# Kernel tuning notes

Hardware: AMD Instinct MI355X
Metric: run time of the kernel (lower is better)

The kernel has to match this reference:

```python
import jax, jax.numpy as jnp
import numpy as np

EPS = 1e-5

def conv1x1(x, w, b):
    # x: [B,Cin,H,W], w: [Cout,Cin], b: [Cout]
    return jnp.einsum('oi,bihw->bohw', w, x) + b[None, :, None, None]

def self_attention(x, qw, qb, kw, kb, vw, vb, fw, fb):
    B, C, H, W = x.shape
    hid = qw.shape[0]
    q = conv1x1(x, qw, qb).reshape(B, hid, H * W).transpose(0, 2, 1)   # [B,HW,hid]
    k = conv1x1(x, kw, kb).reshape(B, hid, H * W)                      # [B,hid,HW]
    v = conv1x1(x, vw, vb).reshape(B, C, H * W)                        # [B,C,HW]
    attn = jax.nn.softmax(jnp.einsum('bnh,bhm->bnm', q, k), axis=-1)   # [B,HW,HW]
    z = jnp.einsum('bnm,bcm->bnc', attn, v)                            # [B,HW,C]
    # faithful to torch .view(B,C,H,W) on contiguous [B,HW,C]: raw reshape, no transpose
    z = z.reshape(B, C, H, W)
    return conv1x1(z * x, fw, fb) + x

def group_norm_per_channel(y, gw, gb):
    # GroupNorm(num_groups == num_channels): per-channel instance norm, biased var
    mean = y.mean(axis=(2, 3), keepdims=True)
    var = ((y - mean) ** 2).mean(axis=(2, 3), keepdims=True)
    yn = (y - mean) * jax.lax.rsqrt(var + EPS)
    return yn * gw[None, :, None, None] + gb[None, :, None, None]

def setup_inputs() -> dict:
    key = jax.random.key(0)
    ks = jax.random.split(key, 32)
    B, C, H, W = 4, 64, 64, 64
    hid, att = 64, 64
    d = {}
    d['x'] = jax.random.normal(ks[0], (B, C, H, W), jnp.float32)
    d['h'] = jax.random.normal(ks[1], (B, hid, H, W), jnp.float32)
    d['c'] = jax.random.normal(ks[2], (B, hid, H, W), jnp.float32)
    i = 3
    for pre, cin in (('ax', C), ('ah', hid)):
        for nm, cout in (('q', att), ('k', att), ('v', cin), ('f', cin)):
            d[f'{pre}_{nm}w'] = jax.random.normal(ks[i], (cout, cin), jnp.float32) * 0.05; i += 1
            d[f'{pre}_{nm}b'] = jax.random.normal(ks[i], (cout,), jnp.float32) * 0.05; i += 1
    d['conv_w'] = jax.random.normal(ks[i], (4 * hid, C + hid, 3, 3), jnp.float32) * 0.05; i += 1
    d['conv_b'] = jax.random.normal(ks[i], (4 * hid,), jnp.float32) * 0.05; i += 1
    d['gn_w'] = jnp.ones((4 * hid,), jnp.float32)
    d['gn_b'] = jnp.zeros((4 * hid,), jnp.float32)
    return d

def reference(x, h, c,
              ax_qw, ax_qb, ax_kw, ax_kb, ax_vw, ax_vb, ax_fw, ax_fb,
              ah_qw, ah_qb, ah_kw, ah_kb, ah_vw, ah_vb, ah_fw, ah_fb,
              conv_w, conv_b, gn_w, gn_b):
    hid = h.shape[1]
    xa = self_attention(x, ax_qw, ax_qb, ax_kw, ax_kb, ax_vw, ax_vb, ax_fw, ax_fb)
    ha = self_attention(h, ah_qw, ah_qb, ah_kw, ah_kb, ah_vw, ah_vb, ah_fw, ah_fb)
    combined = jnp.concatenate([xa, ha], axis=1)
    y = jax.lax.conv_general_dilated(
        combined, conv_w, window_strides=(1, 1), padding=[(1, 1), (1, 1)],
        dimension_numbers=('NCHW', 'OIHW', 'NCHW')) + conv_b[None, :, None, None]
    y = group_norm_per_channel(y, gn_w, gn_b)
    i, f, o, g = jnp.split(y, 4, axis=1)
    i = jax.nn.sigmoid(i); f = jax.nn.sigmoid(f); o = jax.nn.sigmoid(o); g = jnp.tanh(g)
    c_next = f * c + i * g
    h_next = o * jnp.tanh(c_next)
    return jnp.stack([h_next, c_next])  # [2,B,hid,H,W]
```

## Files before the change

### kernel.cpp

```cpp
#include <hip/hip_runtime.h>
#include <hip/hip_bf16.h>


typedef __hip_bfloat16 bf16;
typedef const __hip_bfloat16* bfp;
typedef short bf16x8 __attribute__((ext_vector_type(8)));
typedef short short4v __attribute__((ext_vector_type(4)));
typedef float f32x4 __attribute__((ext_vector_type(4)));
typedef unsigned int u32x4 __attribute__((ext_vector_type(4)));

#define SM_SHIFT 12.0f
#define LOG2E      1.4426950408889634f
#define SM_BIAS2  -17.312340490667562f
#define SM_CLAMP2  86.561702453337805f

__device__ __forceinline__ float ldf(const void* p, long i, int f32) {
    return f32 ? ((const float*)p)[i]
               : __bfloat162float(((const bf16*)p)[i]);
}
__device__ __forceinline__ short f2bf(float f) {
    bf16 h = __float2bfloat16(f);
    return *reinterpret_cast<short*>(&h);
}

__device__ __forceinline__ int sniff_f32(const void* xr)
{
    int lane = threadIdx.x & 63;
    unsigned long long v = ((const unsigned long long*)xr)[lane];
    int ok = 0;
#pragma unroll
    for (int i = 0; i < 4; ++i) {
        int e = (int)((v >> (16 * i + 7)) & 0xFF);
        ok += (e >= 100 && e <= 141);
    }
    ok += __shfl_xor(ok, 1, 64);
    ok += __shfl_xor(ok, 2, 64);
    ok += __shfl_xor(ok, 4, 64);
    ok += __shfl_xor(ok, 8, 64);
    ok += __shfl_xor(ok, 16, 64);
    ok += __shfl_xor(ok, 32, 64);
    return ok < 200;
}

__global__ __launch_bounds__(256) void qkv_kernel(
    const void* __restrict__ Xx, const void* __restrict__ Xh,
    const void* __restrict__ qwx, const void* __restrict__ qbx,
    const void* __restrict__ kwx, const void* __restrict__ kbx,
    const void* __restrict__ vwx, const void* __restrict__ vbx,
    const void* __restrict__ qwh, const void* __restrict__ qbh,
    const void* __restrict__ kwh, const void* __restrict__ kbh,
    const void* __restrict__ vwh, const void* __restrict__ vbh,
    bf16* __restrict__ Qx, bf16* __restrict__ Kx, bf16* __restrict__ Vtx,
    bf16* __restrict__ Qh, bf16* __restrict__ Kh, bf16* __restrict__ Vth,
    const void* __restrict__ cw, bf16* __restrict__ Wt,
    float* __restrict__ gacc, int qkvN)
{
    int bx = blockIdx.x;
    int tid = threadIdx.x;
    int f32 = sniff_f32(Xx);
    if (bx >= qkvN) {
        if (bx == qkvN) {
            for (int j = 0; j < 8; ++j)
                gacc[tid * 8 + j] = 0.f;
        }
        int wi = (bx - qkvN) * 256 + tid;
        int tap = wi >> 15;
        int rem = wi & 32767;
        int oc = rem >> 7, ic = rem & 127;
        Wt[wi] = __float2bfloat16(ldf(cw, ((long)oc * 128 + ic) * 9 + tap, f32));
        return;
    }
    __shared__ __align__(16) short xt[64][72];
    __shared__ __align__(16) short wq[64][72];
    __shared__ __align__(16) short wk[64][72];
    __shared__ __align__(16) short wv[64][72];
    int ab  = (bx >> 8) & 1;
    int idx = bx & 255;
    int b = idx >> 6;
    int n0 = (idx & 63) * 64;
    int wave = tid >> 6, lane = tid & 63;
    int q = lane >> 4, l15 = lane & 15;

    const void* X = ab ? Xh : Xx;
    const void* qw = ab ? qwh : qwx; const void* qb = ab ? qbh : qbx;
    const void* kw = ab ? kwh : kwx; const void* kb = ab ? kbh : kbx;
    const void* vw = ab ? vwh : vwx; const void* vb = ab ? vbh : vbx;
    short* Qg  = (short*)(ab ? Qh  : Qx)  + (long)b * 262144;
    short* Kg  = (short*)(ab ? Kh  : Kx)  + (long)b * 262144;
    short* Vtg = (short*)(ab ? Vth : Vtx) + (long)b * 262144;

    if (!f32) {
        const short* q16 = (const short*)qw;
        const short* k16 = (const short*)kw;
        const short* v16 = (const short*)vw;
        for (int rep = 0; rep < 2; ++rep) {
            int j8 = (rep * 256 + tid) * 8;
            *(bf16x8*)&wq[j8 >> 6][j8 & 63] = *(const bf16x8*)(q16 + j8);
            *(bf16x8*)&wk[j8 >> 6][j8 & 63] = *(const bf16x8*)(k16 + j8);
            *(bf16x8*)&wv[j8 >> 6][j8 & 63] = *(const bf16x8*)(v16 + j8);
        }
    } else {
        for (int rep = 0; rep < 16; ++rep) {
            int j = rep * 256 + tid;
            int i = j >> 6, cc = j & 63;
            wq[i][cc] = f2bf(((const float*)qw)[j]);
            wk[i][cc] = f2bf(((const float*)kw)[j]);
            wv[i][cc] = f2bf(((const float*)vw)[j]);
        }
    }
    long xbase = (long)b * 262144;
    for (int rep = 0; rep < 16; ++rep) {
        int c = rep * 4 + (tid >> 6);
        int p = tid & 63;
        xt[p][c] = f2bf(ldf(X, xbase + (long)c * 4096 + n0 + p, f32));
    }
    __syncthreads();

    bf16x8 a0 = *(const bf16x8*)&xt[wave * 16 + l15][q * 8];
    bf16x8 a1 = *(const bf16x8*)&xt[wave * 16 + l15][32 + q * 8];

    for (int ct = 0; ct < 4; ++ct) {
        bf16x8 bq0 = *(const bf16x8*)&wq[ct * 16 + l15][q * 8];
        bf16x8 bq1 = *(const bf16x8*)&wq[ct * 16 + l15][32 + q * 8];
        f32x4 z = (f32x4){0.f, 0.f, 0.f, 0.f};
        z = __builtin_amdgcn_mfma_f32_16x16x32_bf16(a0, bq0, z, 0, 0, 0);
        z = __builtin_amdgcn_mfma_f32_16x16x32_bf16(a1, bq1, z, 0, 0, 0);
        float bias = ldf(qb, ct * 16 + l15, f32);
        for (int reg = 0; reg < 4; ++reg)
            Qg[(long)(n0 + wave * 16 + q * 4 + reg) * 64 + ct * 16 + l15] =
                f2bf(z[reg] + bias);
    }
    for (int ct = 0; ct < 4; ++ct) {
        bf16x8 bk0 = *(const bf16x8*)&wk[ct * 16 + l15][q * 8];
        bf16x8 bk1 = *(const bf16x8*)&wk[ct * 16 + l15][32 + q * 8];
        f32x4 z = (f32x4){0.f, 0.f, 0.f, 0.f};
        z = __builtin_amdgcn_mfma_f32_16x16x32_bf16(a0, bk0, z, 0, 0, 0);
        z = __builtin_amdgcn_mfma_f32_16x16x32_bf16(a1, bk1, z, 0, 0, 0);
        float bias = ldf(kb, ct * 16 + l15, f32);
        for (int reg = 0; reg < 4; ++reg)
            Kg[(long)(n0 + wave * 16 + q * 4 + reg) * 64 + ct * 16 + l15] =
                f2bf(z[reg] + bias);
    }
    bf16x8 av0 = *(const bf16x8*)&wv[wave * 16 + l15][q * 8];
    bf16x8 av1 = *(const bf16x8*)&wv[wave * 16 + l15][32 + q * 8];
    for (int ct = 0; ct < 4; ++ct) {
        bf16x8 bx0 = *(const bf16x8*)&xt[ct * 16 + l15][q * 8];
        bf16x8 bx1 = *(const bf16x8*)&xt[ct * 16 + l15][32 + q * 8];
        f32x4 z = (f32x4){0.f, 0.f, 0.f, 0.f};
        z = __builtin_amdgcn_mfma_f32_16x16x32_bf16(av0, bx0, z, 0, 0, 0);
        z = __builtin_amdgcn_mfma_f32_16x16x32_bf16(av1, bx1, z, 0, 0, 0);
        for (int reg = 0; reg < 4; ++reg) {
            int c_out = wave * 16 + q * 4 + reg;
            float bias = ldf(vb, c_out, f32);
            Vtg[(long)c_out * 4096 + n0 + ct * 16 + l15] = f2bf(z[reg] + bias);
        }
    }
}

__global__ __launch_bounds__(256, 2) void attn_kernel(
    bfp Qx, bfp Kx, bfp Vtx, bf16* Ox,
    bfp Qh, bfp Kh, bfp Vth, bf16* Oh,
    float* __restrict__ lw, int split)
{
    __shared__ __align__(16) short ks [2][64][64];
    __shared__ __align__(16) short vts[2][64][64];
    int tid = threadIdx.x;
    int wave = tid >> 6, lane = tid & 63;
    int q = lane >> 4, l15 = lane & 15;
    int idx = blockIdx.x & 255;
    int ab, half, mstart, ntile;
    if (split) {
        ab = blockIdx.x >> 9; half = (blockIdx.x >> 8) & 1;
        mstart = half * 2048; ntile = 32;
    } else {
        ab = blockIdx.x >> 8; half = 0; mstart = 0; ntile = 64;
    }
    int b = idx >> 6;
    int rt = idx & 63;
    int n0 = rt * 64 + wave * 16;
    const short* Qb  = (const short*)(ab ? Qh  : Qx)  + (long)b * 262144;
    const short* Kb  = (const short*)(ab ? Kh  : Kx)  + (long)b * 262144;
    const short* Vtb = (const short*)(ab ? Vth : Vtx) + (long)b * 262144;
    short* Ob = (short*)(ab ? Oh : Ox) + (long)half * (1l << 20) + (long)b * 262144;

    bf16x8 aq0 = *(const bf16x8*)(Qb + (long)(n0 + l15) * 64 + q * 8);
    bf16x8 aq1 = *(const bf16x8*)(Qb + (long)(n0 + l15) * 64 + 32 + q * 8);

    f32x4 acc_o[4];
    for (int ct = 0; ct < 4; ++ct) acc_o[ct] = (f32x4){0.f, 0.f, 0.f, 0.f};
    float l_acc = 0.f;

    int swp = (l15 >> 1) & 7;
    int c0 = (q ^ swp) << 3;
    int c1 = ((q + 4) ^ swp) << 3;
    int sw_s = (tid >> 4) & 7;
    int cs = (((tid & 7) ^ sw_s)) << 3;

    int r0 = tid >> 3, r1 = r0 + 32;
    int sr0 = (((r0 >> 5) + (((r0 >> 2) & 1) << 1)) << 4)
            | (((r0 >> 3) & 3) << 2) | (r0 & 3);
    int sr1 = (((r1 >> 5) + (((r1 >> 2) & 1) << 1)) << 4)
            | (((r1 >> 3) & 3) << 2) | (r1 & 3);
    int cs0 = (((tid & 7) ^ ((sr0 >> 1) & 7))) << 3;
    int cs1 = (((tid & 7) ^ ((sr1 >> 1) & 7))) << 3;

    bf16x8 pk0 = *(const bf16x8*)(Kb + (long)(mstart + r0) * 64 + (tid & 7) * 8);
    bf16x8 pk1 = *(const bf16x8*)(Kb + (long)(mstart + r1) * 64 + (tid & 7) * 8);
    bf16x8 pv0 = *(const bf16x8*)(Vtb + (long)r0 * 4096 + mstart + (tid & 7) * 8);
    bf16x8 pv1 = *(const bf16x8*)(Vtb + (long)r1 * 4096 + mstart + (tid & 7) * 8);

    for (int it = 0; it < ntile; ++it) {
        int buf = it & 1;
        *(bf16x8*)&ks[buf][sr0][cs0] = pk0;
        *(bf16x8*)&ks[buf][sr1][cs1] = pk1;
        *(bf16x8*)&vts[buf][r0][cs]  = pv0;
        *(bf16x8*)&vts[buf][r1][cs]  = pv1;
        __syncthreads();
        if (it + 1 < ntile) {
            long m = (long)mstart + (long)(it + 1) * 64;
            pk0 = *(const bf16x8*)(Kb + (m + r0) * 64 + (tid & 7) * 8);
            pk1 = *(const bf16x8*)(Kb + (m + r1) * 64 + (tid & 7) * 8);
            pv0 = *(const bf16x8*)(Vtb + (long)r0 * 4096 + m + (tid & 7) * 8);
            pv1 = *(const bf16x8*)(Vtb + (long)r1 * 4096 + m + (tid & 7) * 8);
        }

        f32x4 s[4];
#pragma unroll
        for (int t = 0; t < 4; ++t) {
            const short* krow = &ks[buf][t * 16 + l15][0];
            bf16x8 ak0 = *(const bf16x8*)(krow + c0);
            bf16x8 ak1 = *(const bf16x8*)(krow + c1);
            f32x4 z = (f32x4){0.f, 0.f, 0.f, 0.f};
            z    = __builtin_amdgcn_mfma_f32_16x16x32_bf16(ak0, aq0, z, 0, 0, 0);
            s[t] = __builtin_amdgcn_mfma_f32_16x16x32_bf16(ak1, aq1, z, 0, 0, 0);
        }

        unsigned P32[8];
        float lt = 0.f;
#pragma unroll
        for (int t = 0; t < 4; ++t) {
            float p0 = __builtin_amdgcn_exp2f(
                fminf(fmaf(s[t][0], LOG2E, SM_BIAS2), SM_CLAMP2));
            float p1 = __builtin_amdgcn_exp2f(
                fminf(fmaf(s[t][1], LOG2E, SM_BIAS2), SM_CLAMP2));
            float p2 = __builtin_amdgcn_exp2f(
                fminf(fmaf(s[t][2], LOG2E, SM_BIAS2), SM_CLAMP2));
            float p3 = __builtin_amdgcn_exp2f(
                fminf(fmaf(s[t][3], LOG2E, SM_BIAS2), SM_CLAMP2));
            lt += (p0 + p1) + (p2 + p3);
            P32[t * 2] = (unsigned)(unsigned short)f2bf(p0)
                       | ((unsigned)(unsigned short)f2bf(p1) << 16);
            P32[t * 2 + 1] = (unsigned)(unsigned short)f2bf(p2)
                           | ((unsigned)(unsigned short)f2bf(p3) << 16);
        }
        l_acc += lt;

        u32x4 B0v = (u32x4){P32[0], P32[1], P32[4], P32[5]};
        u32x4 B1v = (u32x4){P32[2], P32[3], P32[6], P32[7]};
        bf16x8 bp0 = __builtin_bit_cast(bf16x8, B0v);
        bf16x8 bp1 = __builtin_bit_cast(bf16x8, B1v);

        for (int ct = 0; ct < 4; ++ct) {
            const short* vrow = &vts[buf][ct * 16 + l15][0];
            bf16x8 av0 = *(const bf16x8*)(vrow + c0);
            bf16x8 av1 = *(const bf16x8*)(vrow + c1);
            acc_o[ct] = __builtin_amdgcn_mfma_f32_16x16x32_bf16(av0, bp0, acc_o[ct], 0, 0, 0);
            acc_o[ct] = __builtin_amdgcn_mfma_f32_16x16x32_bf16(av1, bp1, acc_o[ct], 0, 0, 0);
        }
    }

    l_acc += __shfl_xor(l_acc, 16, 64);
    l_acc += __shfl_xor(l_acc, 32, 64);

    if (split) {
        if (lane < 16) {
            lw[(long)ab * 32768 + (long)half * 16384
               + (long)b * 4096 + n0 + lane] = l_acc;
        }
        for (int ct = 0; ct < 4; ++ct) {
            short* dst = Ob + (long)(n0 + l15) * 64 + ct * 16 + q * 4;
            dst[0] = f2bf(acc_o[ct][0]);
            dst[1] = f2bf(acc_o[ct][1]);
            dst[2] = f2bf(acc_o[ct][2]);
            dst[3] = f2bf(acc_o[ct][3]);
        }
    } else {
        float iln = 1.f / l_acc;
        for (int ct = 0; ct < 4; ++ct) {
            short* dst = Ob + (long)(n0 + l15) * 64 + ct * 16 + q * 4;
            dst[0] = f2bf(acc_o[ct][0] * iln);
            dst[1] = f2bf(acc_o[ct][1] * iln);
            dst[2] = f2bf(acc_o[ct][2] * iln);
            dst[3] = f2bf(acc_o[ct][3] * iln);
        }
    }
}

__global__ __launch_bounds__(256) void attnout_kernel(
    bfp Ox, const void* __restrict__ Xx,
    const void* __restrict__ fwx, const void* __restrict__ fbx,
    bf16* __restrict__ outx,
    bfp Oh, const void* __restrict__ Xh,
    const void* __restrict__ fwh, const void* __restrict__ fbh,
    bf16* __restrict__ outh,
    const float* __restrict__ lw, int split)
{
    __shared__ __align__(16) short fwt[64][72];
    __shared__ __align__(16) short at [64][72];
    int f32 = sniff_f32(Xx);
    int ab  = blockIdx.x >> 8;
    int idx = blockIdx.x & 255;
    int b = idx >> 6;
    int h = idx & 63;
    int tid = threadIdx.x;
    int wave = tid >> 6, lane = tid & 63;
    int q = lane >> 4, l15 = lane & 15;
    bfp O = ab ? Oh : Ox;
    const void* X = ab ? Xh : Xx;
    const void* fw = ab ? fwh : fwx;
    const void* fb = ab ? fbh : fbx;
    bf16* out = ab ? outh : outx;

    if (!f32) {
        const short* f16p = (const short*)fw;
        for (int rep = 0; rep < 2; ++rep) {
            int j8 = (rep * 256 + tid) * 8;
            *(bf16x8*)&fwt[j8 >> 6][j8 & 63] = *(const bf16x8*)(f16p + j8);
        }
    } else {
        for (int rep = 0; rep < 16; ++rep) {
            int j = rep * 256 + tid;
            fwt[j >> 6][j & 63] = f2bf(((const float*)fw)[j]);
        }
    }
    const bf16* Ob0 = O + (long)b * 262144;
    const bf16* Ob1 = Ob0 + (1l << 20);
    const float* lp0 = lw + (long)ab * 32768 + (long)b * 4096;
    const float* lp1 = lp0 + 16384;
    long xbase = (long)b * 262144;
    {
        int w = tid & 63;
        for (int rep = 0; rep < 16; ++rep) {
            int cn = rep * 4 + (tid >> 6);
            int n = cn * 64 + h;
            float o;
            if (split) {
                float iln = 1.f / (lp0[n] + lp1[n]);
                o = (__bfloat162float(Ob0[(long)n * 64 + w]) +
                     __bfloat162float(Ob1[(long)n * 64 + w])) * iln;
            } else {
                o = __bfloat162float(Ob0[(long)n * 64 + w]);
            }
            float prod = o * ldf(X, xbase + (long)cn * 4096 + h * 64 + w, f32);
            at[w][cn] = f2bf(prod);
        }
    }
    __syncthreads();
    bf16x8 a0 = *(const bf16x8*)&fwt[wave * 16 + l15][q * 8];
    bf16x8 a1 = *(const bf16x8*)&fwt[wave * 16 + l15][32 + q * 8];
    short* outp = (short*)out;
    for (int nt = 0; nt < 4; ++nt) {
        bf16x8 b0 = *(const bf16x8*)&at[nt * 16 + l15][q * 8];
        bf16x8 b1 = *(const bf16x8*)&at[nt * 16 + l15][32 + q * 8];
        f32x4 z = (f32x4){0.f, 0.f, 0.f, 0.f};
        z = __builtin_amdgcn_mfma_f32_16x16x32_bf16(a0, b0, z, 0, 0, 0);
        z = __builtin_amdgcn_mfma_f32_16x16x32_bf16(a1, b1, z, 0, 0, 0);
        int w = nt * 16 + l15;
        short4v o4;
        for (int reg = 0; reg < 4; ++reg) {
            int o = wave * 16 + q * 4 + reg;
            float v = z[reg] + ldf(fb, o, f32) +
                      ldf(X, xbase + (long)o * 4096 + h * 64 + w, f32);
            o4[reg] = f2bf(v);
        }
        *(short4v*)(outp + (((long)(b * 64 + h) * 64 + w) * 64 + wave * 16 + q * 4)) = o4;
    }
}

__global__ __launch_bounds__(256) void conv3x3_kernel(
    bfp xa, bfp ha, bfp Wt, const void* __restrict__ cb,
    bf16* __restrict__ y, float* __restrict__ gacc,
    const void* __restrict__ xraw)
{
    __shared__ __align__(16) short in_s[3][66][136];
    int f32 = sniff_f32(xraw);
    int bx = blockIdx.x;
    int b = bx >> 7;
    int rem = bx & 127;
    int h = rem >> 1;
    int halfoc = rem & 1;
    int tid = threadIdx.x;
    int wave = tid >> 6, lane = tid & 63;
    int q = lane >> 4, l15 = lane & 15;

    const short* xab = (const short*)xa + (long)b * 262144;
    const short* hab = (const short*)ha + (long)b * 262144;
    const bf16x8 zv = {0, 0, 0, 0, 0, 0, 0, 0};
    for (int r = 0; r < 3; ++r) {
        int gy = h + r - 1;
        bool valid = (gy >= 0) && (gy < 64);
        for (int s = 0; s < 2; ++s) {
            int strip = s * 256 + tid;
            int w = strip >> 3;
            int c8 = (strip & 7) * 8;
            bf16x8 vx = zv, vh = zv;
            if (valid) {
                vx = *(const bf16x8*)(xab + ((long)gy * 64 + w) * 64 + c8);
                vh = *(const bf16x8*)(hab + ((long)gy * 64 + w) * 64 + c8);
            }
            *(bf16x8*)&in_s[r][w + 1][c8]      = vx;
            *(bf16x8*)&in_s[r][w + 1][64 + c8] = vh;
        }
    }
    if (tid < 96) {
        int r = tid / 32;
        int rest = tid % 32;
        int col = (rest & 1) ? 65 : 0;
        int c8 = (rest >> 1) * 8;
        *(bf16x8*)&in_s[r][col][c8] = zv;
    }
    __syncthreads();

    int oc0 = halfoc * 128 + wave * 32;
    f32x4 acc[2][4];
    for (int mt = 0; mt < 2; ++mt)
        for (int nt = 0; nt < 4; ++nt)
            acc[mt][nt] = (f32x4){0.f, 0.f, 0.f, 0.f};

    const short* Wb = (const short*)Wt;
    for (int tap = 0; tap < 9; ++tap) {
        int dy = tap / 3, dx = tap - dy * 3;
        for (int kc = 0; kc < 4; ++kc) {
            bf16x8 afrag[2];
            for (int mt = 0; mt < 2; ++mt)
                afrag[mt] = *(const bf16x8*)(
                    Wb + ((long)tap * 256 + oc0 + mt * 16 + l15) * 128 + kc * 32 + q * 8);
            for (int nt = 0; nt < 4; ++nt) {
                bf16x8 bfrag = *(const bf16x8*)&in_s[dy][nt * 16 + l15 + dx][kc * 32 + q * 8];
                for (int mt = 0; mt < 2; ++mt)
                    acc[mt][nt] = __builtin_amdgcn_mfma_f32_16x16x32_bf16(
                        afrag[mt], bfrag, acc[mt][nt], 0, 0, 0);
            }
        }
    }

    long ybase = (long)b * 1048576 + (long)h * 64;
    for (int mt = 0; mt < 2; ++mt) {
        for (int reg = 0; reg < 4; ++reg) {
            int oc = oc0 + mt * 16 + q * 4 + reg;
            float bias = ldf(cb, oc, f32);
            float s = 0.f, s2 = 0.f;
            for (int nt = 0; nt < 4; ++nt) {
                float v = acc[mt][nt][reg] + bias;
                ((short*)y)[ybase + (long)oc * 4096 + nt * 16 + l15] = f2bf(v);
                s += v; s2 = fmaf(v, v, s2);
            }
            s  += __shfl_xor(s,  1, 64);  s2 += __shfl_xor(s2, 1, 64);
            s  += __shfl_xor(s,  2, 64);  s2 += __shfl_xor(s2, 2, 64);
            s  += __shfl_xor(s,  4, 64);  s2 += __shfl_xor(s2, 4, 64);
            s  += __shfl_xor(s,  8, 64);  s2 += __shfl_xor(s2, 8, 64);
            if (l15 == 0) {
                atomicAdd(&gacc[b * 256 + oc], s);
                atomicAdd(&gacc[1024 + b * 256 + oc], s2);
            }
        }
    }
}

__global__ __launch_bounds__(256) void gates_kernel(
    bfp y, const float* __restrict__ gacc,
    const void* __restrict__ gw, const void* __restrict__ gb,
    const void* __restrict__ c_in, void* __restrict__ out)
{
    int f32 = sniff_f32(c_in);
    int idx = blockIdx.x * 256 + threadIdx.x;
    int b = idx >> 18;
    int r = idx & 262143;
    int ch = r >> 12;
    int pix = r & 4095;
    long ybase = (long)b * 1048576;
    float vals[4];
    for (int g = 0; g < 4; ++g) {
        int cc = g * 64 + ch;
        float mu  = gacc[b * 256 + cc] * (1.f / 4096.f);
        float var = gacc[1024 + b * 256 + cc] * (1.f / 4096.f) - mu * mu;
        float rstd = rsqrtf(fmaxf(var, 0.f) + 1e-5f);
        float v = __bfloat162float(y[ybase + (long)cc * 4096 + pix]);
        v = (v - mu) * rstd * ldf(gw, cc, f32) + ldf(gb, cc, f32);
        vals[g] = v;
    }
    float ig = 1.f / (1.f + __expf(-vals[0]));
    float fg = 1.f / (1.f + __expf(-vals[1]));
    float og = 1.f / (1.f + __expf(-vals[2]));
    float gg = tanhf(vals[3]);
    float cprev = ldf(c_in, idx, f32);
    float cn = fg * cprev + ig * gg;
    float hn = og * tanhf(cn);
    if (f32) {
        float* o32 = (float*)out;
        o32[idx] = hn;
        o32[1048576 + idx] = cn;
    } else {
        bf16* o16 = (bf16*)out;
        o16[idx] = __float2bfloat16(hn);
        o16[1048576 + idx] = __float2bfloat16(cn);
    }
}

extern "C" void kernel_launch(void* const* d_in, const int* in_sizes, int n_in,
                              void* d_out, int out_size, void* d_ws, size_t ws_size,
                              hipStream_t stream)
{
    const void* x = d_in[0]; const void* h = d_in[1]; const void* c = d_in[2];
    const void* ax_qw = d_in[3],  *ax_qb = d_in[4];
    const void* ax_kw = d_in[5],  *ax_kb = d_in[6];
    const void* ax_vw = d_in[7],  *ax_vb = d_in[8];
    const void* ax_fw = d_in[9],  *ax_fb = d_in[10];
    const void* ah_qw = d_in[11], *ah_qb = d_in[12];
    const void* ah_kw = d_in[13], *ah_kb = d_in[14];
    const void* ah_vw = d_in[15], *ah_vb = d_in[16];
    const void* ah_fw = d_in[17], *ah_fb = d_in[18];
    const void* conv_w = d_in[19], *conv_b = d_in[20];
    const void* gn_w = d_in[21],  *gn_b = d_in[22];

    char* wsb = (char*)d_ws;
    auto S = [&](int i) { return wsb + ((unsigned long)i << 21); };
    bool splitm = ws_size >= (27ul << 20);
    bool fused  = splitm || ws_size >= (18ul << 20) + 16384;

    bf16* ha = (bf16*)S(0);
    bf16* Wt = (bf16*)S(1);
    bf16 *Qx, *Kx, *Vtx, *Qh, *Kh, *Vth, *xa, *y, *Ox, *Oh;
    char* tail;
    if (splitm) {
        Qx = (bf16*)S(2); Kx = (bf16*)S(3); Vtx = (bf16*)S(4);
        Qh = (bf16*)S(5); Kh = (bf16*)S(6); Vth = (bf16*)S(7);
        xa = (bf16*)S(8);
        Ox = (bf16*)S(9);
        Oh = (bf16*)S(11);
        y = Qx;
        tail = S(13);
    } else if (fused) {
        Qx = (bf16*)S(2); Kx = (bf16*)S(3); Vtx = (bf16*)S(4);
        Qh = (bf16*)S(5); Kh = (bf16*)S(6); Vth = (bf16*)S(7);
        xa = (bf16*)S(8); Ox = Qx; Oh = Qh; y = Qx;
        tail = S(9);
    } else {
        Qx = (bf16*)S(2); Kx = (bf16*)S(3); Vtx = (bf16*)S(4);
        Qh = Qx; Kh = Kx; Vth = Vtx;
        xa = (bf16*)S(6); Ox = Qx; Oh = Qh; y = Qx;
        tail = S(7);
    }
    float* gacc = (float*)tail;
    float* lw   = (float*)(tail + 8192);

    if (fused) {
        qkv_kernel<<<512 + 1152, 256, 0, stream>>>(
            x, h,
            ax_qw, ax_qb, ax_kw, ax_kb, ax_vw, ax_vb,
            ah_qw, ah_qb, ah_kw, ah_kb, ah_vw, ah_vb,
            Qx, Kx, Vtx, Qh, Kh, Vth, conv_w, Wt, gacc, 512);
        if (splitm) {
            attn_kernel<<<1024, 256, 0, stream>>>(
                Qx, Kx, Vtx, Ox, Qh, Kh, Vth, Oh, lw, 1);
            attnout_kernel<<<512, 256, 0, stream>>>(
                Ox, x, ax_fw, ax_fb, xa, Oh, h, ah_fw, ah_fb, ha, lw, 1);
        } else {
            attn_kernel<<<512, 256, 0, stream>>>(
                Qx, Kx, Vtx, Ox, Qh, Kh, Vth, Oh, lw, 0);
            attnout_kernel<<<512, 256, 0, stream>>>(
                Ox, x, ax_fw, ax_fb, xa, Oh, h, ah_fw, ah_fb, ha, lw, 0);
        }
    } else {
        qkv_kernel<<<256 + 1152, 256, 0, stream>>>(
            x, x,
            ax_qw, ax_qb, ax_kw, ax_kb, ax_vw, ax_vb,
            ax_qw, ax_qb, ax_kw, ax_kb, ax_vw, ax_vb,
            Qx, Kx, Vtx, Qx, Kx, Vtx, conv_w, Wt, gacc, 256);
        attn_kernel<<<256, 256, 0, stream>>>(
            Qx, Kx, Vtx, Ox, Qx, Kx, Vtx, Ox, lw, 0);
        attnout_kernel<<<256, 256, 0, stream>>>(
            Ox, x, ax_fw, ax_fb, xa, Ox, x, ax_fw, ax_fb, xa, lw, 0);
        qkv_kernel<<<256, 256, 0, stream>>>(
            h, h,
            ah_qw, ah_qb, ah_kw, ah_kb, ah_vw, ah_vb,
            ah_qw, ah_qb, ah_kw, ah_kb, ah_vw, ah_vb,
            Qh, Kh, Vth, Qh, Kh, Vth, conv_w, Wt, gacc, 256);
        attn_kernel<<<256, 256, 0, stream>>>(
            Qh, Kh, Vth, Oh, Qh, Kh, Vth, Oh, lw, 0);
        attnout_kernel<<<256, 256, 0, stream>>>(
            Oh, h, ah_fw, ah_fb, ha, Oh, h, ah_fw, ah_fb, ha, lw, 0);
    }
    conv3x3_kernel<<<512, 256, 0, stream>>>(xa, ha, Wt, conv_b, y, gacc, x);
    gates_kernel<<<4096, 256, 0, stream>>>(y, gacc, gn_w, gn_b, c, d_out);
}
```

Measured before the change: 222.8 us.

## Switch attention kernel to 32x32x16 MFMA with split-key waves and LDS reduction

Rewrites the attention inner loop to use 32x32x16 bf16 MFMA tiles instead of 16x16x32. The four waves are now arranged as 2 query halves by 2 key halves, with new LDS swizzles to match. Each wave computes partial output and row sums, which are then combined through shared memory before a vectorized store. The larger MFMA shape is meant to cut LDS fragment reads and instruction count per FLOP, at the cost of an extra reduction step, a barrier and a larger accumulator register footprint.

```diff
diff --git a/kernel.cpp b/kernel.cpp
--- a/kernel.cpp
+++ b/kernel.cpp
@@ -7,6 +7,7 @@
 typedef short bf16x8 __attribute__((ext_vector_type(8)));
 typedef short short4v __attribute__((ext_vector_type(4)));
 typedef float f32x4 __attribute__((ext_vector_type(4)));
+typedef float f32x16 __attribute__((ext_vector_type(16)));
 typedef unsigned int u32x4 __attribute__((ext_vector_type(4)));
 
 #define SM_SHIFT 12.0f
@@ -166,7 +167,8 @@
     __shared__ __align__(16) short vts[2][64][64];
     int tid = threadIdx.x;
     int wave = tid >> 6, lane = tid & 63;
-    int q = lane >> 4, l15 = lane & 15;
+    int l31 = lane & 31, hi = lane >> 5;
+    int nh = wave >> 1, mh = wave & 1;
     int idx = blockIdx.x & 255;
     int ab, half, mstart, ntile;
     if (split) {
@@ -177,121 +179,145 @@
     }
     int b = idx >> 6;
     int rt = idx & 63;
-    int n0 = rt * 64 + wave * 16;
+    int n0b = rt * 64;
     const short* Qb  = (const short*)(ab ? Qh  : Qx)  + (long)b * 262144;
     const short* Kb  = (const short*)(ab ? Kh  : Kx)  + (long)b * 262144;
     const short* Vtb = (const short*)(ab ? Vth : Vtx) + (long)b * 262144;
     short* Ob = (short*)(ab ? Oh : Ox) + (long)half * (1l << 20) + (long)b * 262144;
 
-    bf16x8 aq0 = *(const bf16x8*)(Qb + (long)(n0 + l15) * 64 + q * 8);
-    bf16x8 aq1 = *(const bf16x8*)(Qb + (long)(n0 + l15) * 64 + 32 + q * 8);
-
-    f32x4 acc_o[4];
-    for (int ct = 0; ct < 4; ++ct) acc_o[ct] = (f32x4){0.f, 0.f, 0.f, 0.f};
+    int nq = n0b + nh * 32 + l31;
+    bf16x8 aq[4];
+#pragma unroll
+    for (int kc = 0; kc < 4; ++kc)
+        aq[kc] = *(const bf16x8*)(Qb + (long)nq * 64 + kc * 16 + hi * 8);
+
+    f32x16 acc0 = (f32x16)(0.0f);
+    f32x16 acc1 = (f32x16)(0.0f);
     float l_acc = 0.f;
 
-    int swp = (l15 >> 1) & 7;
-    int c0 = (q ^ swp) << 3;
-    int c1 = ((q + 4) ^ swp) << 3;
-    int sw_s = (tid >> 4) & 7;
-    int cs = (((tid & 7) ^ sw_s)) << 3;
+    int sw = (l31 >> 1) & 7;
 
     int r0 = tid >> 3, r1 = r0 + 32;
-    int sr0 = (((r0 >> 5) + (((r0 >> 2) & 1) << 1)) << 4)
-            | (((r0 >> 3) & 3) << 2) | (r0 & 3);
-    int sr1 = (((r1 >> 5) + (((r1 >> 2) & 1) << 1)) << 4)
-            | (((r1 >> 3) & 3) << 2) | (r1 & 3);
-    int cs0 = (((tid & 7) ^ ((sr0 >> 1) & 7))) << 3;
-    int cs1 = (((tid & 7) ^ ((sr1 >> 1) & 7))) << 3;
-
-    bf16x8 pk0 = *(const bf16x8*)(Kb + (long)(mstart + r0) * 64 + (tid & 7) * 8);
-    bf16x8 pk1 = *(const bf16x8*)(Kb + (long)(mstart + r1) * 64 + (tid & 7) * 8);
-    bf16x8 pv0 = *(const bf16x8*)(Vtb + (long)r0 * 4096 + mstart + (tid & 7) * 8);
-    bf16x8 pv1 = *(const bf16x8*)(Vtb + (long)r1 * 4096 + mstart + (tid & 7) * 8);
+    int g = tid & 7;
+    int sr0 = (r0 & 51) | ((r0 & 4) << 1) | ((r0 & 8) >> 1);
+    int sr1 = sr0 + 32;
+    int gk = (g ^ ((sr0 >> 1) & 7)) << 3;
+    int gv = (g ^ ((r0 >> 1) & 7)) << 3;
+
+    bf16x8 pk0 = *(const bf16x8*)(Kb + (long)(mstart + r0) * 64 + g * 8);
+    bf16x8 pk1 = *(const bf16x8*)(Kb + (long)(mstart + r1) * 64 + g * 8);
+    bf16x8 pv0 = *(const bf16x8*)(Vtb + (long)r0 * 4096 + mstart + g * 8);
+    bf16x8 pv1 = *(const bf16x8*)(Vtb + (long)r1 * 4096 + mstart + g * 8);
 
     for (int it = 0; it < ntile; ++it) {
         int buf = it & 1;
-        *(bf16x8*)&ks[buf][sr0][cs0] = pk0;
-        *(bf16x8*)&ks[buf][sr1][cs1] = pk1;
-        *(bf16x8*)&vts[buf][r0][cs]  = pv0;
-        *(bf16x8*)&vts[buf][r1][cs]  = pv1;
+        *(bf16x8*)&ks[buf][sr0][gk] = pk0;
+        *(bf16x8*)&ks[buf][sr1][gk] = pk1;
+        *(bf16x8*)&vts[buf][r0][gv] = pv0;
+        *(bf16x8*)&vts[buf][r1][gv] = pv1;
         __syncthreads();
         if (it + 1 < ntile) {
             long m = (long)mstart + (long)(it + 1) * 64;
-            pk0 = *(const bf16x8*)(Kb + (m + r0) * 64 + (tid & 7) * 8);
-            pk1 = *(const bf16x8*)(Kb + (m + r1) * 64 + (tid & 7) * 8);
-            pv0 = *(const bf16x8*)(Vtb + (long)r0 * 4096 + m + (tid & 7) * 8);
-            pv1 = *(const bf16x8*)(Vtb + (long)r1 * 4096 + m + (tid & 7) * 8);
-        }
-
-        f32x4 s[4];
-#pragma unroll
-        for (int t = 0; t < 4; ++t) {
-            const short* krow = &ks[buf][t * 16 + l15][0];
-            bf16x8 ak0 = *(const bf16x8*)(krow + c0);
-            bf16x8 ak1 = *(const bf16x8*)(krow + c1);
-            f32x4 z = (f32x4){0.f, 0.f, 0.f, 0.f};
-            z    = __builtin_amdgcn_mfma_f32_16x16x32_bf16(ak0, aq0, z, 0, 0, 0);
-            s[t] = __builtin_amdgcn_mfma_f32_16x16x32_bf16(ak1, aq1, z, 0, 0, 0);
+            pk0 = *(const bf16x8*)(Kb + (m + r0) * 64 + g * 8);
+            pk1 = *(const bf16x8*)(Kb + (m + r1) * 64 + g * 8);
+            pv0 = *(const bf16x8*)(Vtb + (long)r0 * 4096 + m + g * 8);
+            pv1 = *(const bf16x8*)(Vtb + (long)r1 * 4096 + m + g * 8);
+        }
+
+        f32x16 s = (f32x16)(0.0f);
+        const short* kbase = &ks[buf][mh * 32 + l31][0];
+#pragma unroll
+        for (int kc = 0; kc < 4; ++kc) {
+            bf16x8 ak = *(const bf16x8*)(kbase + (((kc * 2 + hi) ^ sw) << 3));
+            s = __builtin_amdgcn_mfma_f32_32x32x16_bf16(ak, aq[kc], s, 0, 0, 0);
         }
 
         unsigned P32[8];
         float lt = 0.f;
 #pragma unroll
-        for (int t = 0; t < 4; ++t) {
+        for (int i = 0; i < 8; ++i) {
             float p0 = __builtin_amdgcn_exp2f(
-                fminf(fmaf(s[t][0], LOG2E, SM_BIAS2), SM_CLAMP2));
+                fminf(fmaf(s[2 * i], LOG2E, SM_BIAS2), SM_CLAMP2));
             float p1 = __builtin_amdgcn_exp2f(
-                fminf(fmaf(s[t][1], LOG2E, SM_BIAS2), SM_CLAMP2));
-            float p2 = __builtin_amdgcn_exp2f(
-                fminf(fmaf(s[t][2], LOG2E, SM_BIAS2), SM_CLAMP2));
-            float p3 = __builtin_amdgcn_exp2f(
-                fminf(fmaf(s[t][3], LOG2E, SM_BIAS2), SM_CLAMP2));
-            lt += (p0 + p1) + (p2 + p3);
-            P32[t * 2] = (unsigned)(unsigned short)f2bf(p0)
-                       | ((unsigned)(unsigned short)f2bf(p1) << 16);
-            P32[t * 2 + 1] = (unsigned)(unsigned short)f2bf(p2)
-                           | ((unsigned)(unsigned short)f2bf(p3) << 16);
+                fminf(fmaf(s[2 * i + 1], LOG2E, SM_BIAS2), SM_CLAMP2));
+            lt += p0 + p1;
+            P32[i] = (unsigned)(unsigned short)f2bf(p0)
+                   | ((unsigned)(unsigned short)f2bf(p1) << 16);
         }
         l_acc += lt;
-
-        u32x4 B0v = (u32x4){P32[0], P32[1], P32[4], P32[5]};
-        u32x4 B1v = (u32x4){P32[2], P32[3], P32[6], P32[7]};
+        u32x4 B0v = (u32x4){P32[0], P32[1], P32[2], P32[3]};
+        u32x4 B1v = (u32x4){P32[4], P32[5], P32[6], P32[7]};
         bf16x8 bp0 = __builtin_bit_cast(bf16x8, B0v);
         bf16x8 bp1 = __builtin_bit_cast(bf16x8, B1v);
 
-        for (int ct = 0; ct < 4; ++ct) {
-            const short* vrow = &vts[buf][ct * 16 + l15][0];
-            bf16x8 av0 = *(const bf16x8*)(vrow + c0);
-            bf16x8 av1 = *(const bf16x8*)(vrow + c1);
-            acc_o[ct] = __builtin_amdgcn_mfma_f32_16x16x32_bf16(av0, bp0, acc_o[ct], 0, 0, 0);
-            acc_o[ct] = __builtin_amdgcn_mfma_f32_16x16x32_bf16(av1, bp1, acc_o[ct], 0, 0, 0);
-        }
-    }
-
-    l_acc += __shfl_xor(l_acc, 16, 64);
+        const short* v0base = &vts[buf][l31][0];
+        const short* v1base = &vts[buf][32 + l31][0];
+#pragma unroll
+        for (int mc = 0; mc < 2; ++mc) {
+            int gm = ((mh * 4 + mc * 2 + hi) ^ sw) << 3;
+            bf16x8 av0 = *(const bf16x8*)(v0base + gm);
+            bf16x8 av1 = *(const bf16x8*)(v1base + gm);
+            bf16x8 bp = mc ? bp1 : bp0;
+            acc0 = __builtin_amdgcn_mfma_f32_32x32x16_bf16(av0, bp, acc0, 0, 0, 0);
+            acc1 = __builtin_amdgcn_mfma_f32_32x32x16_bf16(av1, bp, acc1, 0, 0, 0);
+        }
+    }
+
     l_acc += __shfl_xor(l_acc, 32, 64);
 
-    if (split) {
-        if (lane < 16) {
-            lw[(long)ab * 32768 + (long)half * 16384
-               + (long)b * 4096 + n0 + lane] = l_acc;
-        }
-        for (int ct = 0; ct < 4; ++ct) {
-            short* dst = Ob + (long)(n0 + l15) * 64 + ct * 16 + q * 4;
-            dst[0] = f2bf(acc_o[ct][0]);
-            dst[1] = f2bf(acc_o[ct][1]);
-            dst[2] = f2bf(acc_o[ct][2]);
-            dst[3] = f2bf(acc_o[ct][3]);
-        }
-    } else {
-        float iln = 1.f / l_acc;
-        for (int ct = 0; ct < 4; ++ct) {
-            short* dst = Ob + (long)(n0 + l15) * 64 + ct * 16 + q * 4;
-            dst[0] = f2bf(acc_o[ct][0] * iln);
-            dst[1] = f2bf(acc_o[ct][1] * iln);
-            dst[2] = f2bf(acc_o[ct][2] * iln);
-            dst[3] = f2bf(acc_o[ct][3] * iln);
+    __syncthreads();
+    float* fs = (float*)&ks[0][0][0];
+    float* fl = fs + 4096;
+    if (mh == 1) {
+#pragma unroll
+        for (int r = 0; r < 16; ++r) {
+            int row = (r & 3) + ((r >> 2) << 3) + (hi << 2);
+            fs[nh * 2048 + row * 32 + l31]        = acc0[r];
+            fs[nh * 2048 + 1024 + row * 32 + l31] = acc1[r];
+        }
+        if (lane < 32) fl[nh * 32 + l31] = l_acc;
+    }
+    __syncthreads();
+    if (mh == 0) {
+        float l_tot = l_acc + fl[nh * 32 + l31];
+#pragma unroll
+        for (int r = 0; r < 16; ++r) {
+            int row = (r & 3) + ((r >> 2) << 3) + (hi << 2);
+            acc0[r] += fs[nh * 2048 + row * 32 + l31];
+            acc1[r] += fs[nh * 2048 + 1024 + row * 32 + l31];
+        }
+        int n = n0b + nh * 32 + l31;
+        short* dst = Ob + (long)n * 64;
+        if (split) {
+            if (lane < 32)
+                lw[(long)ab * 32768 + (long)half * 16384
+                   + (long)b * 4096 + n] = l_tot;
+#pragma unroll
+            for (int rq = 0; rq < 4; ++rq) {
+                int c0 = (rq << 3) + (hi << 2);
+                short4v o4a, o4b;
+#pragma unroll
+                for (int j = 0; j < 4; ++j) {
+                    o4a[j] = f2bf(acc0[rq * 4 + j]);
+                    o4b[j] = f2bf(acc1[rq * 4 + j]);
+                }
+                *(short4v*)(dst + c0)      = o4a;
+                *(short4v*)(dst + 32 + c0) = o4b;
+            }
+        } else {
+            float iln = 1.f / l_tot;
+#pragma unroll
+            for (int rq = 0; rq < 4; ++rq) {
+                int c0 = (rq << 3) + (hi << 2);
+                short4v o4a, o4b;
+#pragma unroll
+                for (int j = 0; j < 4; ++j) {
+                    o4a[j] = f2bf(acc0[rq * 4 + j] * iln);
+                    o4b[j] = f2bf(acc1[rq * 4 + j] * iln);
+                }
+                *(short4v*)(dst + c0)      = o4a;
+                *(short4v*)(dst + 32 + c0) = o4b;
+            }
         }
     }
 }
```

Result: no change. 225.1 us (+1.0%).
